# Kernel tuning notes

Measured on AMD Instinct MI355X. Metric: run time of the kernel, lower is better.

The kernel has to match this reference:

```python
import jax, jax.numpy as jnp
import numpy as np

H, D_MODEL, LEN_Q, LEN_K, D_K, D_V = 16, 1024, 2048, 2048, 64, 64
BATCH = 4
SCALE = 1.0 / np.sqrt(float(D_K))


def setup_inputs() -> dict:
    key = jax.random.key(0)
    ks = jax.random.split(key, 10)
    inp = {
        "Q": jax.random.normal(ks[0], (BATCH, LEN_Q, D_MODEL), dtype=jnp.float32),
        "K": jax.random.normal(ks[1], (BATCH, LEN_K, D_MODEL), dtype=jnp.float32),
        "V": jax.random.normal(ks[2], (BATCH, LEN_K, D_MODEL), dtype=jnp.float32),
        "mask": jax.random.randint(ks[3], (BATCH, LEN_K), 0, 2, dtype=jnp.int32),
        # Linear params (torch Linear: y = x @ W.T + b); store W as [in, out].
        "Wq": jax.random.normal(ks[4], (D_MODEL, H * D_K), dtype=jnp.float32) * (1.0 / np.sqrt(D_MODEL)),
        "bq": jnp.zeros((H * D_K,), dtype=jnp.float32),
        "Wk": jax.random.normal(ks[5], (D_MODEL, H * D_K), dtype=jnp.float32) * (1.0 / np.sqrt(D_MODEL)),
        "bk": jnp.zeros((H * D_K,), dtype=jnp.float32),
        "Wv": jax.random.normal(ks[6], (D_MODEL, H * D_V), dtype=jnp.float32) * (1.0 / np.sqrt(D_MODEL)),
        "bv": jnp.zeros((H * D_V,), dtype=jnp.float32),
    }
    return inp


def reference(Q, K, V, mask, Wq, bq, Wk, bk, Wv, bv):
    B = Q.shape[0]
    # Projections -> [B, S, H, d]
    q = (Q @ Wq + bq).reshape(B, LEN_Q, H, D_K)
    k = (K @ Wk + bk).reshape(B, LEN_K, H, D_K)
    v = (V @ Wv + bv).reshape(B, LEN_K, H, D_V)
    # Scores: [B, H, len_q, len_k]
    scores = jnp.einsum("bqhd,bkhd->bhqk", q, k) * SCALE
    # Key-padding mask broadcast over heads and queries
    scores = jnp.where(mask[:, None, None, :] == 0, jnp.float32(-1e9), scores)
    alpha = jax.nn.softmax(scores, axis=-1)
    out = jnp.einsum("bhqk,bkhd->bqhd", alpha, v)  # [B, len_q, H, d_v]
    return out.reshape(B, LEN_Q, H * D_V)
```

## Files before the change

### kernel.cpp

```cpp
#include <hip/hip_runtime.h>

#define NH 16
#define DM 1024
#define SQ 2048
#define BT 4

typedef __attribute__((ext_vector_type(8))) short bf16x8;
typedef __attribute__((ext_vector_type(4))) short sh4;
typedef __attribute__((ext_vector_type(4))) float f4;
typedef __attribute__((ext_vector_type(4))) float fv4;
typedef unsigned short u16;

#define M2BIAS 23.083120654f
#define SCALE2 0.18033688f

__device__ __forceinline__ u16 f2bf(float f) {
    union { float f; unsigned u; } v; v.f = f;
    unsigned r = v.u + 0x7FFFu + ((v.u >> 16) & 1u);
    return (u16)(r >> 16);
}

__device__ __forceinline__ float fast_exp2(float x) {
#if __has_builtin(__builtin_amdgcn_exp2f)
    return __builtin_amdgcn_exp2f(x);
#else
    return exp2f(x);
#endif
}

#define GLD16(gp, lp) __builtin_amdgcn_global_load_lds( \
    (const __attribute__((address_space(1))) void*)(gp), \
    (__attribute__((address_space(3))) void*)(lp), 16, 0, 0)

__global__ __launch_bounds__(256) void cvt_x(const float* __restrict__ x, u16* __restrict__ y) {
    int i = blockIdx.x * 256 + threadIdx.x;
    fv4 v = ((const fv4*)x)[i];
    sh4 r;
    r[0] = (short)f2bf(v[0]); r[1] = (short)f2bf(v[1]);
    r[2] = (short)f2bf(v[2]); r[3] = (short)f2bf(v[3]);
    ((sh4*)y)[i] = r;
}

__global__ __launch_bounds__(256) void cvt_wT(const float* __restrict__ Wsrc, u16* __restrict__ Wt) {
    __shared__ float t[64][65];
    int r0 = blockIdx.x * 64, c0 = blockIdx.y * 64;
    #pragma unroll
    for (int i = 0; i < 16; ++i) {
        int idx = i * 256 + threadIdx.x;
        int r = idx >> 6, c = idx & 63;
        t[r][c] = Wsrc[(size_t)(r0 + r) * DM + c0 + c];
    }
    __syncthreads();
    #pragma unroll
    for (int i = 0; i < 16; ++i) {
        int idx = i * 256 + threadIdx.x;
        int n = idx >> 6, k = idx & 63;
        Wt[(size_t)(c0 + n) * DM + r0 + k] = f2bf(t[k][n]);
    }
}

__global__ __launch_bounds__(256) void mk_mbias(const int* __restrict__ mask, float* __restrict__ mb) {
    int i = blockIdx.x * 256 + threadIdx.x;
    mb[i] = mask[i] ? -M2BIAS : -__builtin_inff();
}

__global__ __launch_bounds__(256) void gemm_proj(const u16* __restrict__ A, const u16* __restrict__ Bt,
                                                 const float* __restrict__ bias, u16* __restrict__ outp,
                                                 int vmode) {
    __shared__ u16 As[128 * 64];
    __shared__ u16 Bs[128 * 64];
    int tid = threadIdx.x;
    int w = tid >> 6, lane = tid & 63, quad = lane >> 4, l16 = lane & 15;
    int wm = w >> 1, wn = w & 1;
    int r8 = lane >> 3, cg = (lane & 7) ^ r8;
    const u16* Ag = A + (size_t)blockIdx.x * 128 * DM;
    const u16* Bg = Bt + (size_t)blockIdx.y * 128 * DM;

    f4 acc[4][4];
    #pragma unroll
    for (int mt = 0; mt < 4; ++mt)
        #pragma unroll
        for (int nt = 0; nt < 4; ++nt) acc[mt][nt] = f4{0.f, 0.f, 0.f, 0.f};

    for (int kt = 0; kt < 16; ++kt) {
        int kofs = kt * 64 + cg * 8;
        #pragma unroll
        for (int c = 0; c < 4; ++c) {
            int rbase = w * 32 + c * 8;
            GLD16(Ag + (size_t)(rbase + r8) * DM + kofs, &As[rbase * 64]);
            GLD16(Bg + (size_t)(rbase + r8) * DM + kofs, &Bs[rbase * 64]);
        }
        __syncthreads();
        #pragma unroll
        for (int ks = 0; ks < 2; ++ks) {
            bf16x8 afr[4], bfr[4];
            #pragma unroll
            for (int mt = 0; mt < 4; ++mt) {
                int row = wm * 64 + mt * 16 + l16;
                int ch = (ks * 4 + quad) ^ (row & 7);
                afr[mt] = *(const bf16x8*)&As[row * 64 + ch * 8];
            }
            #pragma unroll
            for (int nt = 0; nt < 4; ++nt) {
                int row = wn * 64 + nt * 16 + l16;
                int ch = (ks * 4 + quad) ^ (row & 7);
                bfr[nt] = *(const bf16x8*)&Bs[row * 64 + ch * 8];
            }
            #pragma unroll
            for (int mt = 0; mt < 4; ++mt)
                #pragma unroll
                for (int nt = 0; nt < 4; ++nt)
                    acc[mt][nt] = __builtin_amdgcn_mfma_f32_16x16x32_bf16(afr[mt], bfr[nt], acc[mt][nt], 0, 0, 0);
        }
        __syncthreads();
    }

    #pragma unroll
    for (int nt = 0; nt < 4; ++nt) {
        int ncol = blockIdx.y * 128 + wn * 64 + nt * 16 + l16;
        float bn = bias[ncol];
        int h = ncol >> 6, d = ncol & 63;
        #pragma unroll
        for (int mt = 0; mt < 4; ++mt) {
            int mbase = blockIdx.x * 128 + wm * 64 + mt * 16 + quad * 4;
            int bidx = mbase >> 11, s0 = mbase & 2047;
            if (vmode == 0) {
                size_t base = ((size_t)bidx * NH + h) * SQ;
                #pragma unroll
                for (int reg = 0; reg < 4; ++reg)
                    outp[(base + s0 + reg) * 64 + d] = f2bf(acc[mt][nt][reg] + bn);
            } else {
                sh4 pk;
                #pragma unroll
                for (int reg = 0; reg < 4; ++reg) pk[reg] = (short)f2bf(acc[mt][nt][reg] + bn);
                *(sh4*)&outp[(((size_t)bidx * NH + h) * 64 + d) * SQ + s0] = pk;
            }
        }
    }
}

__device__ __forceinline__ float redsum16(float v) {
    v += __shfl_xor(v, 1); v += __shfl_xor(v, 2);
    v += __shfl_xor(v, 4); v += __shfl_xor(v, 8);
    return v;
}

__global__ __launch_bounds__(256, 3) void attn(const u16* __restrict__ qw, const u16* __restrict__ kw,
                                               const u16* __restrict__ vtw, const float* __restrict__ mbias,
                                               float* __restrict__ outp) {
    __shared__ u16 Ks[2][64 * 64];
    __shared__ u16 Vs[2][64 * 64];
    __shared__ short P[4][32 * 72];
    int tid = threadIdx.x;
    int w = tid >> 6, lane = tid & 63, quad = lane >> 4, l16 = lane & 15;
    int r8 = lane >> 3, sl = lane & 7;
    int bh = blockIdx.y, b = bh >> 4, h = bh & 15;
    int qbase = blockIdx.x * 128 + w * 32;
    const u16* qp = qw + (size_t)bh * SQ * 64;
    const u16* kp = kw + (size_t)bh * SQ * 64;
    const u16* vp = vtw + (size_t)bh * 64 * SQ;
    const float* mbp = mbias + b * SQ;
    short* Pw = (short*)P[w];

    bf16x8 aq[2][2];
    #pragma unroll
    for (int mt = 0; mt < 2; ++mt)
        #pragma unroll
        for (int ks = 0; ks < 2; ++ks)
            aq[mt][ks] = *(const bf16x8*)&qp[(size_t)(qbase + mt * 16 + l16) * 64 + ks * 32 + quad * 8];

    f4 o[2][4];
    float lrow[2][4];
    #pragma unroll
    for (int mt = 0; mt < 2; ++mt) {
        #pragma unroll
        for (int nt = 0; nt < 4; ++nt) o[mt][nt] = f4{0.f, 0.f, 0.f, 0.f};
        #pragma unroll
        for (int reg = 0; reg < 4; ++reg) lrow[mt][reg] = 0.f;
    }

    auto stage = [&](int buf, int k0) {
        #pragma unroll
        for (int j = 0; j < 2; ++j) {
            int row = w * 16 + j * 8 + r8;
            int gsl = sl ^ (row & 7);
            GLD16(kp + (size_t)(k0 + row) * 64 + gsl * 8, &Ks[buf][(w * 16 + j * 8) * 64]);
            GLD16(vp + (size_t)row * SQ + k0 + gsl * 8, &Vs[buf][(w * 16 + j * 8) * 64]);
        }
    };

    stage(0, 0);
    for (int kb = 0; kb < 32; ++kb) {
        int buf = kb & 1;
        int k0 = kb * 64;
        __syncthreads();
        if (kb + 1 < 32) stage(buf ^ 1, k0 + 64);

        bf16x8 bk[4][2];
        #pragma unroll
        for (int nt = 0; nt < 4; ++nt)
            #pragma unroll
            for (int ks = 0; ks < 2; ++ks) {
                int r = nt * 16 + l16;
                int slot = (ks * 4 + quad) ^ (r & 7);
                bk[nt][ks] = *(const bf16x8*)&Ks[buf][r * 64 + slot * 8];
            }
        f4 S[2][4];
        #pragma unroll
        for (int mt = 0; mt < 2; ++mt)
            #pragma unroll
            for (int nt = 0; nt < 4; ++nt) {
                f4 s = f4{0.f, 0.f, 0.f, 0.f};
                s = __builtin_amdgcn_mfma_f32_16x16x32_bf16(aq[mt][0], bk[nt][0], s, 0, 0, 0);
                s = __builtin_amdgcn_mfma_f32_16x16x32_bf16(aq[mt][1], bk[nt][1], s, 0, 0, 0);
                S[mt][nt] = s;
            }
        float bias2[4];
        #pragma unroll
        for (int nt = 0; nt < 4; ++nt)
            bias2[nt] = mbp[k0 + nt * 16 + l16];
        #pragma unroll
        for (int mt = 0; mt < 2; ++mt)
            #pragma unroll
            for (int nt = 0; nt < 4; ++nt) {
                #pragma unroll
                for (int reg = 0; reg < 4; ++reg) {
                    float p = fast_exp2(S[mt][nt][reg] * SCALE2 + bias2[nt]);
                    lrow[mt][reg] += p;
                    Pw[(mt * 16 + quad * 4 + reg) * 72 + nt * 16 + l16] =
                        (short)(__float_as_uint(p) >> 16);
                }
            }
        #pragma unroll
        for (int kk = 0; kk < 2; ++kk) {
            bf16x8 ap[2], bv[4];
            #pragma unroll
            for (int mt = 0; mt < 2; ++mt)
                ap[mt] = *(const bf16x8*)&Pw[(mt * 16 + l16) * 72 + kk * 32 + quad * 8];
            #pragma unroll
            for (int nt = 0; nt < 4; ++nt) {
                int d = nt * 16 + l16;
                int slot = (kk * 4 + quad) ^ (d & 7);
                bv[nt] = *(const bf16x8*)&Vs[buf][d * 64 + slot * 8];
            }
            #pragma unroll
            for (int mt = 0; mt < 2; ++mt)
                #pragma unroll
                for (int nt = 0; nt < 4; ++nt)
                    o[mt][nt] = __builtin_amdgcn_mfma_f32_16x16x32_bf16(ap[mt], bv[nt], o[mt][nt], 0, 0, 0);
        }
    }

    #pragma unroll
    for (int mt = 0; mt < 2; ++mt)
        #pragma unroll
        for (int reg = 0; reg < 4; ++reg) {
            float inv = 1.f / redsum16(lrow[mt][reg]);
            int row = qbase + mt * 16 + quad * 4 + reg;
            size_t obase = ((size_t)b * SQ + row) * DM + h * 64;
            #pragma unroll
            for (int nt = 0; nt < 4; ++nt)
                outp[obase + nt * 16 + l16] = o[mt][nt][reg] * inv;
        }
}

extern "C" void kernel_launch(void* const* d_in, const int* in_sizes, int n_in,
                              void* d_out, int out_size, void* d_ws, size_t ws_size,
                              hipStream_t stream) {
    (void)in_sizes; (void)n_in; (void)out_size; (void)ws_size;
    const float* Q  = (const float*)d_in[0];
    const float* K  = (const float*)d_in[1];
    const float* V  = (const float*)d_in[2];
    const int* mask = (const int*)d_in[3];
    const float* Wq = (const float*)d_in[4];
    const float* bq = (const float*)d_in[5];
    const float* Wk = (const float*)d_in[6];
    const float* bk = (const float*)d_in[7];
    const float* Wv = (const float*)d_in[8];
    const float* bv = (const float*)d_in[9];
    float* out = (float*)d_out;
    char* ws = (char*)d_ws;
    u16* q_ws = (u16*)(ws);
    u16* k_ws = (u16*)(ws + (size_t)16 * 1024 * 1024);
    u16* v_ws = (u16*)(ws + (size_t)32 * 1024 * 1024);
    u16* xbuf = (u16*)(ws + (size_t)48 * 1024 * 1024);
    u16* wbuf = (u16*)(ws + (size_t)64 * 1024 * 1024);
    float* mb = (float*)(ws + (size_t)48 * 1024 * 1024);

    dim3 gGemm(64, 8), gW(16, 16);
    cvt_x<<<8192, 256, 0, stream>>>(Q, xbuf);
    cvt_wT<<<gW, 256, 0, stream>>>(Wq, wbuf);
    gemm_proj<<<gGemm, 256, 0, stream>>>(xbuf, wbuf, bq, q_ws, 0);
    cvt_x<<<8192, 256, 0, stream>>>(K, xbuf);
    cvt_wT<<<gW, 256, 0, stream>>>(Wk, wbuf);
    gemm_proj<<<gGemm, 256, 0, stream>>>(xbuf, wbuf, bk, k_ws, 0);
    cvt_x<<<8192, 256, 0, stream>>>(V, xbuf);
    cvt_wT<<<gW, 256, 0, stream>>>(Wv, wbuf);
    gemm_proj<<<gGemm, 256, 0, stream>>>(xbuf, wbuf, bv, v_ws, 1);
    mk_mbias<<<32, 256, 0, stream>>>(mask, mb);
    attn<<<dim3(16, 64), 256, 0, stream>>>(q_ws, k_ws, v_ws, mb, out);
}
```

Measured before the change: 362.0 us.

## Transpose QK^T MFMA to pack P stores and interleave softmax with PV

QK^T MFMA operands are swapped so each lane holds four consecutive keys of one query row. This allows vectorized mask-bias loads and packed 4-element P writes to shared memory, replacing scalar stores. The exp/pack of P is split per kk half and interleaved with the PV MFMAs. The row-sum reduction moves to the epilogue via cross-quad shuffles. The grid is also swapped so consecutive blocks share a query-block index across heads, and the loop is unrolled by two, which may raise register pressure.

```diff
diff --git a/kernel.cpp b/kernel.cpp
--- a/kernel.cpp
+++ b/kernel.cpp
@@ -139,12 +139,6 @@
     }
 }
 
-__device__ __forceinline__ float redsum16(float v) {
-    v += __shfl_xor(v, 1); v += __shfl_xor(v, 2);
-    v += __shfl_xor(v, 4); v += __shfl_xor(v, 8);
-    return v;
-}
-
 __global__ __launch_bounds__(256, 3) void attn(const u16* __restrict__ qw, const u16* __restrict__ kw,
                                                const u16* __restrict__ vtw, const float* __restrict__ mbias,
                                                float* __restrict__ outp) {
@@ -154,8 +148,9 @@
     int tid = threadIdx.x;
     int w = tid >> 6, lane = tid & 63, quad = lane >> 4, l16 = lane & 15;
     int r8 = lane >> 3, sl = lane & 7;
-    int bh = blockIdx.y, b = bh >> 4, h = bh & 15;
-    int qbase = blockIdx.x * 128 + w * 32;
+    int bh = blockIdx.x, b = bh >> 4;
+    int h = bh & 15;
+    int qbase = blockIdx.y * 128 + w * 32;
     const u16* qp = qw + (size_t)bh * SQ * 64;
     const u16* kp = kw + (size_t)bh * SQ * 64;
     const u16* vp = vtw + (size_t)bh * 64 * SQ;
@@ -170,13 +165,12 @@
             aq[mt][ks] = *(const bf16x8*)&qp[(size_t)(qbase + mt * 16 + l16) * 64 + ks * 32 + quad * 8];
 
     f4 o[2][4];
-    float lrow[2][4];
+    float lrow[2][2];
     #pragma unroll
     for (int mt = 0; mt < 2; ++mt) {
         #pragma unroll
         for (int nt = 0; nt < 4; ++nt) o[mt][nt] = f4{0.f, 0.f, 0.f, 0.f};
-        #pragma unroll
-        for (int reg = 0; reg < 4; ++reg) lrow[mt][reg] = 0.f;
+        lrow[mt][0] = 0.f; lrow[mt][1] = 0.f;
     }
 
     auto stage = [&](int buf, int k0) {
@@ -190,53 +184,39 @@
     };
 
     stage(0, 0);
+    #pragma unroll 2
     for (int kb = 0; kb < 32; ++kb) {
         int buf = kb & 1;
         int k0 = kb * 64;
         __syncthreads();
+        fv4 bias4[4];
+        #pragma unroll
+        for (int kt = 0; kt < 4; ++kt)
+            bias4[kt] = *(const fv4*)&mbp[k0 + kt * 16 + quad * 4];
         if (kb + 1 < 32) stage(buf ^ 1, k0 + 64);
 
         bf16x8 bk[4][2];
         #pragma unroll
-        for (int nt = 0; nt < 4; ++nt)
+        for (int kt = 0; kt < 4; ++kt)
             #pragma unroll
             for (int ks = 0; ks < 2; ++ks) {
-                int r = nt * 16 + l16;
+                int r = kt * 16 + l16;
                 int slot = (ks * 4 + quad) ^ (r & 7);
-                bk[nt][ks] = *(const bf16x8*)&Ks[buf][r * 64 + slot * 8];
-            }
-        f4 S[2][4];
-        #pragma unroll
-        for (int mt = 0; mt < 2; ++mt)
-            #pragma unroll
-            for (int nt = 0; nt < 4; ++nt) {
+                bk[kt][ks] = *(const bf16x8*)&Ks[buf][r * 64 + slot * 8];
+            }
+        f4 S[4][2];
+        #pragma unroll
+        for (int kt = 0; kt < 4; ++kt)
+            #pragma unroll
+            for (int mt = 0; mt < 2; ++mt) {
                 f4 s = f4{0.f, 0.f, 0.f, 0.f};
-                s = __builtin_amdgcn_mfma_f32_16x16x32_bf16(aq[mt][0], bk[nt][0], s, 0, 0, 0);
-                s = __builtin_amdgcn_mfma_f32_16x16x32_bf16(aq[mt][1], bk[nt][1], s, 0, 0, 0);
-                S[mt][nt] = s;
-            }
-        float bias2[4];
-        #pragma unroll
-        for (int nt = 0; nt < 4; ++nt)
-            bias2[nt] = mbp[k0 + nt * 16 + l16];
-        #pragma unroll
-        for (int mt = 0; mt < 2; ++mt)
-            #pragma unroll
-            for (int nt = 0; nt < 4; ++nt) {
-                #pragma unroll
-                for (int reg = 0; reg < 4; ++reg) {
-                    float p = fast_exp2(S[mt][nt][reg] * SCALE2 + bias2[nt]);
-                    lrow[mt][reg] += p;
-                    Pw[(mt * 16 + quad * 4 + reg) * 72 + nt * 16 + l16] =
-                        (short)(__float_as_uint(p) >> 16);
-                }
+                s = __builtin_amdgcn_mfma_f32_16x16x32_bf16(bk[kt][0], aq[mt][0], s, 0, 0, 0);
+                s = __builtin_amdgcn_mfma_f32_16x16x32_bf16(bk[kt][1], aq[mt][1], s, 0, 0, 0);
+                S[kt][mt] = s;
             }
         #pragma unroll
         for (int kk = 0; kk < 2; ++kk) {
-            bf16x8 ap[2], bv[4];
-            #pragma unroll
-            for (int mt = 0; mt < 2; ++mt)
-                ap[mt] = *(const bf16x8*)&Pw[(mt * 16 + l16) * 72 + kk * 32 + quad * 8];
+            bf16x8 bv[4];
             #pragma unroll
             for (int nt = 0; nt < 4; ++nt) {
                 int d = nt * 16 + l16;
@@ -244,6 +224,27 @@
                 bv[nt] = *(const bf16x8*)&Vs[buf][d * 64 + slot * 8];
             }
             #pragma unroll
+            for (int kt = kk * 2; kt < kk * 2 + 2; ++kt)
+                #pragma unroll
+                for (int mt = 0; mt < 2; ++mt) {
+                    f4 s = S[kt][mt];
+                    float p0 = fast_exp2(s[0] * SCALE2 + bias4[kt][0]);
+                    float p1 = fast_exp2(s[1] * SCALE2 + bias4[kt][1]);
+                    float p2 = fast_exp2(s[2] * SCALE2 + bias4[kt][2]);
+                    float p3 = fast_exp2(s[3] * SCALE2 + bias4[kt][3]);
+                    lrow[mt][kk] += (p0 + p1) + (p2 + p3);
+                    sh4 pk;
+                    pk[0] = (short)(__float_as_uint(p0) >> 16);
+                    pk[1] = (short)(__float_as_uint(p1) >> 16);
+                    pk[2] = (short)(__float_as_uint(p2) >> 16);
+                    pk[3] = (short)(__float_as_uint(p3) >> 16);
+                    *(sh4*)&Pw[(mt * 16 + l16) * 72 + kt * 16 + quad * 4] = pk;
+                }
+            bf16x8 ap[2];
+            #pragma unroll
+            for (int mt = 0; mt < 2; ++mt)
+                ap[mt] = *(const bf16x8*)&Pw[(mt * 16 + l16) * 72 + kk * 32 + quad * 8];
+            #pragma unroll
             for (int mt = 0; mt < 2; ++mt)
                 #pragma unroll
                 for (int nt = 0; nt < 4; ++nt)
@@ -252,16 +253,20 @@
     }
 
     #pragma unroll
-    for (int mt = 0; mt < 2; ++mt)
+    for (int mt = 0; mt < 2; ++mt) {
+        float v = lrow[mt][0] + lrow[mt][1];
+        v += __shfl_xor(v, 16);
+        v += __shfl_xor(v, 32);
         #pragma unroll
         for (int reg = 0; reg < 4; ++reg) {
-            float inv = 1.f / redsum16(lrow[mt][reg]);
+            float inv = 1.f / __shfl(v, quad * 4 + reg);
             int row = qbase + mt * 16 + quad * 4 + reg;
             size_t obase = ((size_t)b * SQ + row) * DM + h * 64;
             #pragma unroll
             for (int nt = 0; nt < 4; ++nt)
                 outp[obase + nt * 16 + l16] = o[mt][nt][reg] * inv;
         }
+    }
 }
 
 extern "C" void kernel_launch(void* const* d_in, const int* in_sizes, int n_in,
@@ -298,5 +303,5 @@
     cvt_wT<<<gW, 256, 0, stream>>>(Wv, wbuf);
     gemm_proj<<<gGemm, 256, 0, stream>>>(xbuf, wbuf, bv, v_ws, 1);
     mk_mbias<<<32, 256, 0, stream>>>(mask, mb);
-    attn<<<dim3(16, 64), 256, 0, stream>>>(q_ws, k_ws, v_ws, mb, out);
-}
+    attn<<<dim3(64, 16), 256, 0, stream>>>(q_ws, k_ws, v_ws, mb, out);
+}
```

Measured after the change: 369.4 us. +2.0%, slower.
